# Optimization experiments

Measured on AMD Instinct MI355X. Metric: run time of the kernel, lower is better.

Reference implementation:

```python
import jax, jax.numpy as jnp
import numpy as np

EPS = 1e-6  # torch F.pairwise_distance eps, added to the difference elementwise

B, Z = 8192, 128
N_CLASSES = 62
P = int(N_CLASSES * 1.5)  # 93 proxies


def pdist(a, b):
    """||a_i - b_j + EPS||_2 for all pairs, without a [N,M,Z] intermediate.
    Expansion: ||a-b||^2 + 2*EPS*sum(a-b) + Z*EPS^2."""
    aa = jnp.sum(a * a, axis=-1)[:, None]
    bb = jnp.sum(b * b, axis=-1)[None, :]
    ab = a @ b.T
    eps_term = 2.0 * EPS * (jnp.sum(a, -1)[:, None] - jnp.sum(b, -1)[None, :]) + a.shape[-1] * EPS * EPS
    return jnp.sqrt(jnp.maximum(aa + bb - 2.0 * ab + eps_term, 0.0))


def setup_inputs() -> dict:
    key = jax.random.key(0)
    k0, k1, k2 = jax.random.split(key, 3)
    z = jax.random.normal(k0, (B, Z), dtype=jnp.float32)
    y_idx = jax.random.randint(k1, (B,), 0, N_CLASSES, dtype=jnp.int32)
    proxies = jax.random.uniform(k2, (P, Z), dtype=jnp.float32)  # nn.init.uniform_
    y_map = jnp.arange(N_CLASSES, dtype=jnp.int32)  # y_to_relative_y_train (unique classes)
    return {"z": z, "y_idx": y_idx, "proxies": proxies, "y_map": y_map}


def reference(z, y_idx, proxies, y_map):
    # F.normalize(proxies, p=2, dim=-1) with 1e-12 clamp
    prx = proxies / jnp.maximum(jnp.linalg.norm(proxies, axis=-1, keepdims=True), 1e-12)
    # y_rel[j] = position where y_to_relative_y_train == y_idx[j] (exactly one match)
    y_rel = jnp.argmax(y_map[None, :] == y_idx[:, None], axis=-1)  # [B]

    anchors = np.arange(0, z.shape[0] - 3, 3)  # static anchor indices i
    z_a = z[anchors]                            # [A,Z]

    # nearest proxy to each anchor
    D_prox = pdist(z_a, prx)                    # [A,P]
    prox_p = prx[jnp.argmin(D_prox, axis=-1)]   # [A,Z]

    # distance from chosen proxy to every sample; restrict to suffix j>=i with same class
    D_pz = pdist(prox_p, z)                     # [A,B]
    mask = (np.arange(z.shape[0])[None, :] >= anchors[:, None]) & \
           (y_rel[None, :] == y_rel[anchors][:, None])  # [A,B], row i always has j=i True
    D_pos = jnp.where(mask, D_pz, -jnp.inf)
    j_p = jnp.argmax(D_pos, axis=-1)            # hardest positive index
    D_p = jnp.take_along_axis(D_pos, j_p[:, None], axis=-1)[:, 0]  # [A]

    # distances from hardest positive to all proxies -> NCA denominator
    D_n = pdist(z[j_p], prx)                    # [A,P]
    losses = D_p + jax.nn.logsumexp(-D_n, axis=-1)  # -log(exp(-D_p)/sum exp(-D_n))
    return jnp.mean(losses)
```

## Files before the change

### kernel.cpp

```cpp
#include <hip/hip_runtime.h>
#include <math.h>

#define B_N   8192
#define Z_D   128
#define P_N   93
#define NCLS  62
#define A_N   2730
#define BCAP  256
#define GT_S  96
#define NPART 683
#define TWO_EPS   2e-6f
#define ZEPS2     (128.0f * 1e-6f * 1e-6f)

__device__ __forceinline__ float wave_sum(float v) {
#pragma unroll
  for (int off = 1; off < 64; off <<= 1) v += __shfl_xor(v, off, 64);
  return v;
}
__device__ __forceinline__ float wave_min(float v) {
#pragma unroll
  for (int off = 1; off < 64; off <<= 1) v = fminf(v, __shfl_xor(v, off, 64));
  return v;
}

__global__ __launch_bounds__(512) void kA(
    const float* __restrict__ z, const int* __restrict__ y_idx,
    const float* __restrict__ prox, const int* __restrict__ y_map,
    float* __restrict__ pp, float* __restrict__ sp,
    float* __restrict__ zz, float* __restrict__ sz,
    int* __restrict__ cnt, int2* __restrict__ bkt, float* __restrict__ GT) {
  __shared__ float linv[6];
  __shared__ int lmem[BCAP];
  __shared__ int lcnt;
  const int b = blockIdx.x, tid = threadIdx.x;
  const int lane = tid & 63, wv = tid >> 6;

  if (b < 256) {
    const int jch = b & 15, kt = b >> 4, k0 = kt * 6;
    const int nk = (kt == 15) ? 3 : 6;
    const int j = jch * 512 + tid;
    const float* __restrict__ zrow = z + (size_t)j * Z_D;
    if (wv < nk) {
      const int k = k0 + wv;
      const float a = prox[k * Z_D + lane];
      const float c = prox[k * Z_D + 64 + lane];
      const float s = wave_sum(a + c);
      const float q = wave_sum(a * a + c * c);
      const float inv = 1.0f / fmaxf(sqrtf(q), 1e-12f);
      if (lane == 0) {
        linv[wv] = inv;
        if (jch == 0) { pp[k] = q * inv * inv; sp[k] = s * inv; }
      }
    }
    __syncthreads();
    if (kt < 15) {
      const float* __restrict__ p0 = prox + (size_t)(k0 + 0) * Z_D;
      const float* __restrict__ p1 = prox + (size_t)(k0 + 1) * Z_D;
      const float* __restrict__ p2 = prox + (size_t)(k0 + 2) * Z_D;
      const float* __restrict__ p3 = prox + (size_t)(k0 + 3) * Z_D;
      const float* __restrict__ p4 = prox + (size_t)(k0 + 4) * Z_D;
      const float* __restrict__ p5 = prox + (size_t)(k0 + 5) * Z_D;
      float a0 = 0, a1 = 0, a2 = 0, a3 = 0, a4 = 0, a5 = 0;
#pragma unroll 8
      for (int i4 = 0; i4 < Z_D; i4 += 4) {
        const float4 zv = *(const float4*)(zrow + i4);
        const float4 q0 = *(const float4*)(p0 + i4);
        const float4 q1 = *(const float4*)(p1 + i4);
        const float4 q2 = *(const float4*)(p2 + i4);
        const float4 q3 = *(const float4*)(p3 + i4);
        const float4 q4 = *(const float4*)(p4 + i4);
        const float4 q5 = *(const float4*)(p5 + i4);
        a0 += zv.x * q0.x + zv.y * q0.y + zv.z * q0.z + zv.w * q0.w;
        a1 += zv.x * q1.x + zv.y * q1.y + zv.z * q1.z + zv.w * q1.w;
        a2 += zv.x * q2.x + zv.y * q2.y + zv.z * q2.z + zv.w * q2.w;
        a3 += zv.x * q3.x + zv.y * q3.y + zv.z * q3.z + zv.w * q3.w;
        a4 += zv.x * q4.x + zv.y * q4.y + zv.z * q4.z + zv.w * q4.w;
        a5 += zv.x * q5.x + zv.y * q5.y + zv.z * q5.z + zv.w * q5.w;
      }
      const float v0 = linv[0], v1 = linv[1], v2 = linv[2];
      const float v3 = linv[3], v4 = linv[4], v5 = linv[5];
      float* g = GT + (size_t)j * GT_S + k0;
      *(float2*)(g + 0) = make_float2(a0 * v0, a1 * v1);
      *(float2*)(g + 2) = make_float2(a2 * v2, a3 * v3);
      *(float2*)(g + 4) = make_float2(a4 * v4, a5 * v5);
    } else {
      const float* __restrict__ p0 = prox + (size_t)90 * Z_D;
      const float* __restrict__ p1 = prox + (size_t)91 * Z_D;
      const float* __restrict__ p2 = prox + (size_t)92 * Z_D;
      float a0 = 0, a1 = 0, a2 = 0, zs = 0, zq = 0;
#pragma unroll 8
      for (int i4 = 0; i4 < Z_D; i4 += 4) {
        const float4 zv = *(const float4*)(zrow + i4);
        const float4 q0 = *(const float4*)(p0 + i4);
        const float4 q1 = *(const float4*)(p1 + i4);
        const float4 q2 = *(const float4*)(p2 + i4);
        zs += zv.x + zv.y + zv.z + zv.w;
        zq += zv.x * zv.x + zv.y * zv.y + zv.z * zv.z + zv.w * zv.w;
        a0 += zv.x * q0.x + zv.y * q0.y + zv.z * q0.z + zv.w * q0.w;
        a1 += zv.x * q1.x + zv.y * q1.y + zv.z * q1.z + zv.w * q1.w;
        a2 += zv.x * q2.x + zv.y * q2.y + zv.z * q2.z + zv.w * q2.w;
      }
      float* g = GT + (size_t)j * GT_S + 90;
      *(float2*)(g) = make_float2(a0 * linv[0], a1 * linv[1]);
      g[2] = a2 * linv[2];
      zz[j] = zq;
      sz[j] = zs;
    }
  } else {
    const int c = b - 256;
    if (tid == 0) lcnt = 0;
    __syncthreads();
    const int ym = y_map[c];
    for (int j = tid; j < B_N; j += 512) {
      if (y_idx[j] == ym) {
        const int pos = atomicAdd(&lcnt, 1);
        if (pos < BCAP) lmem[pos] = j;
      }
    }
    __syncthreads();
    const int n = min(lcnt, BCAP);
    if (tid == 0) cnt[c] = n;
    for (int m = wv; m < n; m += 8) {
      const int j = lmem[m];
      const float a = z[(size_t)j * Z_D + lane];
      const float c2 = z[(size_t)j * Z_D + 64 + lane];
      const float s = wave_sum(a + c2);
      const float q = wave_sum(a * a + c2 * c2);
      if (lane == 0)
        bkt[c * BCAP + m] = make_int2(j, __float_as_int(q - TWO_EPS * s));
    }
  }
}

__global__ __launch_bounds__(256) void kB2(
    const int* __restrict__ y_idx, const int* __restrict__ y_map,
    const float* __restrict__ pp, const float* __restrict__ sp,
    const float* __restrict__ zz, const float* __restrict__ sz,
    const int* __restrict__ cnt, const int2* __restrict__ bkt,
    const float* __restrict__ GT, float* __restrict__ partial) {
  __shared__ float lpp[P_N], lsp[P_N];
  __shared__ int lymap[NCLS];
  __shared__ float part[4];
  const int tid = threadIdx.x, lane = tid & 63, wv = tid >> 6;
  if (tid < P_N) { lpp[tid] = pp[tid]; lsp[tid] = sp[tid]; }
  if (tid < NCLS) lymap[tid] = y_map[tid];
  __syncthreads();

  const int wid = blockIdx.x * 4 + wv;
  float loss = 0.0f;
  if (wid < A_N) {
    const int i = 3 * wid;
    const int yi = y_idx[i];
    const unsigned long long mm = __ballot(lane < NCLS && lymap[lane] == yi);
    const int cls = __ffsll(mm) - 1;
    const float zzi = zz[i], szi = sz[i];
    const int kB = lane + 64;

    const float* __restrict__ GTi = GT + (size_t)i * GT_S;
    float v1 = fmaxf(zzi + lpp[lane] - 2.0f * GTi[lane] +
                     TWO_EPS * (szi - lsp[lane]) + ZEPS2, 0.0f);
    int i1 = lane;
    if (kB < P_N) {
      const float v2 = fmaxf(zzi + lpp[kB] - 2.0f * GTi[kB] +
                             TWO_EPS * (szi - lsp[kB]) + ZEPS2, 0.0f);
      if (v2 < v1) { v1 = v2; i1 = kB; }
    }
#pragma unroll
    for (int off = 1; off < 64; off <<= 1) {
      const float ov = __shfl_xor(v1, off, 64);
      const int oi = __shfl_xor(i1, off, 64);
      if (ov < v1 || (ov == v1 && oi < i1)) { v1 = ov; i1 = oi; }
    }
    const int p = i1;

    const float cp = lpp[p] + TWO_EPS * lsp[p] + ZEPS2;
    const int n = cnt[cls];
    const int2* __restrict__ bk = bkt + cls * BCAP;
    float best = -INFINITY;
    int bestj = 0x7fffffff;
    for (int t = lane; t < n; t += 64) {
      const int2 e = bk[t];
      const int jj = e.x;
      if (jj >= i) {
        const float vv = fmaxf(cp + __int_as_float(e.y) -
                               2.0f * GT[(size_t)jj * GT_S + p], 0.0f);
        if (vv > best || (vv == best && jj < bestj)) { best = vv; bestj = jj; }
      }
    }
#pragma unroll
    for (int off = 1; off < 64; off <<= 1) {
      const float ov = __shfl_xor(best, off, 64);
      const int oj = __shfl_xor(bestj, off, 64);
      if (ov > best || (ov == best && oj < bestj)) { best = ov; bestj = oj; }
    }
    const float Dp = sqrtf(best);
    const int jp = bestj;

    const float zzj = zz[jp], szj = sz[jp];
    const float* __restrict__ GTj = GT + (size_t)jp * GT_S;
    const float d1 = sqrtf(fmaxf(zzj + lpp[lane] - 2.0f * GTj[lane] +
                                 TWO_EPS * (szj - lsp[lane]) + ZEPS2, 0.0f));
    float d2 = INFINITY;
    if (kB < P_N)
      d2 = sqrtf(fmaxf(zzj + lpp[kB] - 2.0f * GTj[kB] +
                       TWO_EPS * (szj - lsp[kB]) + ZEPS2, 0.0f));
    const float mn = wave_min(fminf(d1, d2));
    float ss = expf(mn - d1) + ((kB < P_N) ? expf(mn - d2) : 0.0f);
    ss = wave_sum(ss);
    loss = Dp - mn + logf(ss);
  }
  if (lane == 0) part[wv] = (wid < A_N) ? loss : 0.0f;
  __syncthreads();
  if (tid == 0)
    partial[blockIdx.x] = part[0] + part[1] + part[2] + part[3];
}

__global__ __launch_bounds__(256) void kC2(const float* __restrict__ partial,
                                           float* __restrict__ out) {
  __shared__ float ps[4];
  const int tid = threadIdx.x, lane = tid & 63, wv = tid >> 6;
  float s = 0.0f;
  for (int i = tid; i < NPART; i += 256) s += partial[i];
  s = wave_sum(s);
  if (lane == 0) ps[wv] = s;
  __syncthreads();
  if (tid == 0)
    out[0] = (ps[0] + ps[1] + ps[2] + ps[3]) * (1.0f / (float)A_N);
}

extern "C" void kernel_launch(void* const* d_in, const int* in_sizes, int n_in,
                              void* d_out, int out_size, void* d_ws, size_t ws_size,
                              hipStream_t stream) {
  const float* z = (const float*)d_in[0];
  const int* y_idx = (const int*)d_in[1];
  const float* prox = (const float*)d_in[2];
  const int* y_map = (const int*)d_in[3];
  float* out = (float*)d_out;

  char* ws = (char*)d_ws;
  float* pp    = (float*)(ws + 0);
  float* sp    = (float*)(ws + 512);
  float* zz    = (float*)(ws + 1024);
  float* sz    = (float*)(ws + 33792);
  int*   cnt   = (int*)  (ws + 66560);
  int2*  bkt   = (int2*) (ws + 66816);
  float* parts = (float*)(ws + 193792);
  float* GT    = (float*)(ws + 196608);

  kA<<<256 + NCLS, 512, 0, stream>>>(z, y_idx, prox, y_map,
                                     pp, sp, zz, sz, cnt, bkt, GT);
  kB2<<<NPART, 256, 0, stream>>>(y_idx, y_map, pp, sp, zz, sz,
                                 cnt, bkt, GT, parts);
  kC2<<<1, 256, 0, stream>>>(parts, out);
}
```

Baseline: 90.93 us.

## Fuse final reduction via atomics, 2 rows per thread in kA, prefetch bucket loads

Removes the third reduction kernel. kB2 blocks instead add their partial sums into a global accumulator, and the last block, found with an atomic counter, writes the mean. kA is halved to 256 threads with each thread computing two z rows, which reuses the proxy loads. The bucket scan in kB2 is unrolled into four prefetched loads so the GT gathers can overlap. This saves one launch and exposes more memory-level parallelism, but the float atomics make the summation order nondeterministic, and the accumulator is reset in kA, which relies on kernel ordering.

```diff
diff --git a/kernel.cpp b/kernel.cpp
--- a/kernel.cpp
+++ b/kernel.cpp
@@ -12,6 +12,9 @@
 #define TWO_EPS   2e-6f
 #define ZEPS2     (128.0f * 1e-6f * 1e-6f)
 
+#define AT_ADDU(p, v) __hip_atomic_fetch_add((p), (v), __ATOMIC_RELAXED, __HIP_MEMORY_SCOPE_AGENT)
+#define AT_ADDF(p, v) __hip_atomic_fetch_add((p), (v), __ATOMIC_RELAXED, __HIP_MEMORY_SCOPE_AGENT)
+
 __device__ __forceinline__ float wave_sum(float v) {
 #pragma unroll
   for (int off = 1; off < 64; off <<= 1) v += __shfl_xor(v, off, 64);
@@ -23,36 +26,40 @@
   return v;
 }
 
-__global__ __launch_bounds__(512) void kA(
+__global__ __launch_bounds__(256) void kA(
     const float* __restrict__ z, const int* __restrict__ y_idx,
     const float* __restrict__ prox, const int* __restrict__ y_map,
     float* __restrict__ pp, float* __restrict__ sp,
     float* __restrict__ zz, float* __restrict__ sz,
-    int* __restrict__ cnt, int2* __restrict__ bkt, float* __restrict__ GT) {
+    int* __restrict__ cnt, int2* __restrict__ bkt, float* __restrict__ GT,
+    float* __restrict__ accf, unsigned int* __restrict__ bar) {
   __shared__ float linv[6];
   __shared__ int lmem[BCAP];
   __shared__ int lcnt;
   const int b = blockIdx.x, tid = threadIdx.x;
   const int lane = tid & 63, wv = tid >> 6;
 
+  if (b == 0 && tid == 0) { accf[0] = 0.0f; bar[0] = 0u; }
+
   if (b < 256) {
     const int jch = b & 15, kt = b >> 4, k0 = kt * 6;
     const int nk = (kt == 15) ? 3 : 6;
-    const int j = jch * 512 + tid;
-    const float* __restrict__ zrow = z + (size_t)j * Z_D;
-    if (wv < nk) {
-      const int k = k0 + wv;
+    for (int r = wv; r < nk; r += 4) {
+      const int k = k0 + r;
       const float a = prox[k * Z_D + lane];
       const float c = prox[k * Z_D + 64 + lane];
       const float s = wave_sum(a + c);
       const float q = wave_sum(a * a + c * c);
       const float inv = 1.0f / fmaxf(sqrtf(q), 1e-12f);
       if (lane == 0) {
-        linv[wv] = inv;
+        linv[r] = inv;
         if (jch == 0) { pp[k] = q * inv * inv; sp[k] = s * inv; }
       }
     }
     __syncthreads();
+    const int j0 = jch * 512 + tid, j1 = j0 + 256;
+    const float* __restrict__ zr0 = z + (size_t)j0 * Z_D;
+    const float* __restrict__ zr1 = z + (size_t)j1 * Z_D;
     if (kt < 15) {
       const float* __restrict__ p0 = prox + (size_t)(k0 + 0) * Z_D;
       const float* __restrict__ p1 = prox + (size_t)(k0 + 1) * Z_D;
@@ -61,57 +68,79 @@
       const float* __restrict__ p4 = prox + (size_t)(k0 + 4) * Z_D;
       const float* __restrict__ p5 = prox + (size_t)(k0 + 5) * Z_D;
       float a0 = 0, a1 = 0, a2 = 0, a3 = 0, a4 = 0, a5 = 0;
+      float b0 = 0, b1 = 0, b2 = 0, b3 = 0, b4 = 0, b5 = 0;
 #pragma unroll 8
       for (int i4 = 0; i4 < Z_D; i4 += 4) {
-        const float4 zv = *(const float4*)(zrow + i4);
+        const float4 z0 = *(const float4*)(zr0 + i4);
+        const float4 z1 = *(const float4*)(zr1 + i4);
         const float4 q0 = *(const float4*)(p0 + i4);
         const float4 q1 = *(const float4*)(p1 + i4);
         const float4 q2 = *(const float4*)(p2 + i4);
         const float4 q3 = *(const float4*)(p3 + i4);
         const float4 q4 = *(const float4*)(p4 + i4);
         const float4 q5 = *(const float4*)(p5 + i4);
-        a0 += zv.x * q0.x + zv.y * q0.y + zv.z * q0.z + zv.w * q0.w;
-        a1 += zv.x * q1.x + zv.y * q1.y + zv.z * q1.z + zv.w * q1.w;
-        a2 += zv.x * q2.x + zv.y * q2.y + zv.z * q2.z + zv.w * q2.w;
-        a3 += zv.x * q3.x + zv.y * q3.y + zv.z * q3.z + zv.w * q3.w;
-        a4 += zv.x * q4.x + zv.y * q4.y + zv.z * q4.z + zv.w * q4.w;
-        a5 += zv.x * q5.x + zv.y * q5.y + zv.z * q5.z + zv.w * q5.w;
+        a0 += z0.x * q0.x + z0.y * q0.y + z0.z * q0.z + z0.w * q0.w;
+        a1 += z0.x * q1.x + z0.y * q1.y + z0.z * q1.z + z0.w * q1.w;
+        a2 += z0.x * q2.x + z0.y * q2.y + z0.z * q2.z + z0.w * q2.w;
+        a3 += z0.x * q3.x + z0.y * q3.y + z0.z * q3.z + z0.w * q3.w;
+        a4 += z0.x * q4.x + z0.y * q4.y + z0.z * q4.z + z0.w * q4.w;
+        a5 += z0.x * q5.x + z0.y * q5.y + z0.z * q5.z + z0.w * q5.w;
+        b0 += z1.x * q0.x + z1.y * q0.y + z1.z * q0.z + z1.w * q0.w;
+        b1 += z1.x * q1.x + z1.y * q1.y + z1.z * q1.z + z1.w * q1.w;
+        b2 += z1.x * q2.x + z1.y * q2.y + z1.z * q2.z + z1.w * q2.w;
+        b3 += z1.x * q3.x + z1.y * q3.y + z1.z * q3.z + z1.w * q3.w;
+        b4 += z1.x * q4.x + z1.y * q4.y + z1.z * q4.z + z1.w * q4.w;
+        b5 += z1.x * q5.x + z1.y * q5.y + z1.z * q5.z + z1.w * q5.w;
       }
       const float v0 = linv[0], v1 = linv[1], v2 = linv[2];
       const float v3 = linv[3], v4 = linv[4], v5 = linv[5];
-      float* g = GT + (size_t)j * GT_S + k0;
-      *(float2*)(g + 0) = make_float2(a0 * v0, a1 * v1);
-      *(float2*)(g + 2) = make_float2(a2 * v2, a3 * v3);
-      *(float2*)(g + 4) = make_float2(a4 * v4, a5 * v5);
+      float* g0 = GT + (size_t)j0 * GT_S + k0;
+      float* g1 = GT + (size_t)j1 * GT_S + k0;
+      *(float2*)(g0 + 0) = make_float2(a0 * v0, a1 * v1);
+      *(float2*)(g0 + 2) = make_float2(a2 * v2, a3 * v3);
+      *(float2*)(g0 + 4) = make_float2(a4 * v4, a5 * v5);
+      *(float2*)(g1 + 0) = make_float2(b0 * v0, b1 * v1);
+      *(float2*)(g1 + 2) = make_float2(b2 * v2, b3 * v3);
+      *(float2*)(g1 + 4) = make_float2(b4 * v4, b5 * v5);
     } else {
       const float* __restrict__ p0 = prox + (size_t)90 * Z_D;
       const float* __restrict__ p1 = prox + (size_t)91 * Z_D;
       const float* __restrict__ p2 = prox + (size_t)92 * Z_D;
-      float a0 = 0, a1 = 0, a2 = 0, zs = 0, zq = 0;
+      float a0 = 0, a1 = 0, a2 = 0, b0 = 0, b1 = 0, b2 = 0;
+      float s0 = 0, q0s = 0, s1 = 0, q1s = 0;
 #pragma unroll 8
       for (int i4 = 0; i4 < Z_D; i4 += 4) {
-        const float4 zv = *(const float4*)(zrow + i4);
+        const float4 z0 = *(const float4*)(zr0 + i4);
+        const float4 z1 = *(const float4*)(zr1 + i4);
         const float4 q0 = *(const float4*)(p0 + i4);
         const float4 q1 = *(const float4*)(p1 + i4);
         const float4 q2 = *(const float4*)(p2 + i4);
-        zs += zv.x + zv.y + zv.z + zv.w;
-        zq += zv.x * zv.x + zv.y * zv.y + zv.z * zv.z + zv.w * zv.w;
-        a0 += zv.x * q0.x + zv.y * q0.y + zv.z * q0.z + zv.w * q0.w;
-        a1 += zv.x * q1.x + zv.y * q1.y + zv.z * q1.z + zv.w * q1.w;
-        a2 += zv.x * q2.x + zv.y * q2.y + zv.z * q2.z + zv.w * q2.w;
-      }
-      float* g = GT + (size_t)j * GT_S + 90;
-      *(float2*)(g) = make_float2(a0 * linv[0], a1 * linv[1]);
-      g[2] = a2 * linv[2];
-      zz[j] = zq;
-      sz[j] = zs;
+        s0 += z0.x + z0.y + z0.z + z0.w;
+        q0s += z0.x * z0.x + z0.y * z0.y + z0.z * z0.z + z0.w * z0.w;
+        s1 += z1.x + z1.y + z1.z + z1.w;
+        q1s += z1.x * z1.x + z1.y * z1.y + z1.z * z1.z + z1.w * z1.w;
+        a0 += z0.x * q0.x + z0.y * q0.y + z0.z * q0.z + z0.w * q0.w;
+        a1 += z0.x * q1.x + z0.y * q1.y + z0.z * q1.z + z0.w * q1.w;
+        a2 += z0.x * q2.x + z0.y * q2.y + z0.z * q2.z + z0.w * q2.w;
+        b0 += z1.x * q0.x + z1.y * q0.y + z1.z * q0.z + z1.w * q0.w;
+        b1 += z1.x * q1.x + z1.y * q1.y + z1.z * q1.z + z1.w * q1.w;
+        b2 += z1.x * q2.x + z1.y * q2.y + z1.z * q2.z + z1.w * q2.w;
+      }
+      float* g0 = GT + (size_t)j0 * GT_S + 90;
+      float* g1 = GT + (size_t)j1 * GT_S + 90;
+      *(float2*)(g0) = make_float2(a0 * linv[0], a1 * linv[1]);
+      g0[2] = a2 * linv[2];
+      *(float2*)(g1) = make_float2(b0 * linv[0], b1 * linv[1]);
+      g1[2] = b2 * linv[2];
+      zz[j0] = q0s; sz[j0] = s0;
+      zz[j1] = q1s; sz[j1] = s1;
     }
   } else {
     const int c = b - 256;
     if (tid == 0) lcnt = 0;
     __syncthreads();
     const int ym = y_map[c];
-    for (int j = tid; j < B_N; j += 512) {
+    for (int j = tid; j < B_N; j += 256) {
       if (y_idx[j] == ym) {
         const int pos = atomicAdd(&lcnt, 1);
         if (pos < BCAP) lmem[pos] = j;
@@ -120,7 +149,7 @@
     __syncthreads();
     const int n = min(lcnt, BCAP);
     if (tid == 0) cnt[c] = n;
-    for (int m = wv; m < n; m += 8) {
+    for (int m = wv; m < n; m += 4) {
       const int j = lmem[m];
       const float a = z[(size_t)j * Z_D + lane];
       const float c2 = z[(size_t)j * Z_D + 64 + lane];
@@ -137,7 +166,8 @@
     const float* __restrict__ pp, const float* __restrict__ sp,
     const float* __restrict__ zz, const float* __restrict__ sz,
     const int* __restrict__ cnt, const int2* __restrict__ bkt,
-    const float* __restrict__ GT, float* __restrict__ partial) {
+    const float* __restrict__ GT, float* accf, unsigned int* bar,
+    float* __restrict__ out) {
   __shared__ float lpp[P_N], lsp[P_N];
   __shared__ int lymap[NCLS];
   __shared__ float part[4];
@@ -176,14 +206,25 @@
     const float cp = lpp[p] + TWO_EPS * lsp[p] + ZEPS2;
     const int n = cnt[cls];
     const int2* __restrict__ bk = bkt + cls * BCAP;
+    int2 e[4];
+    float gg[4];
+#pragma unroll
+    for (int r = 0; r < 4; ++r) {
+      const int t = lane + r * 64;
+      e[r] = (t < n) ? bk[t] : make_int2(-1, 0);
+    }
+#pragma unroll
+    for (int r = 0; r < 4; ++r) {
+      const int row = (e[r].x >= i) ? e[r].x : i;
+      gg[r] = GT[(size_t)row * GT_S + p];
+    }
     float best = -INFINITY;
     int bestj = 0x7fffffff;
-    for (int t = lane; t < n; t += 64) {
-      const int2 e = bk[t];
-      const int jj = e.x;
+#pragma unroll
+    for (int r = 0; r < 4; ++r) {
+      const int jj = e[r].x;
       if (jj >= i) {
-        const float vv = fmaxf(cp + __int_as_float(e.y) -
-                               2.0f * GT[(size_t)jj * GT_S + p], 0.0f);
+        const float vv = fmaxf(cp + __int_as_float(e[r].y) - 2.0f * gg[r], 0.0f);
         if (vv > best || (vv == best && jj < bestj)) { best = vv; bestj = jj; }
       }
     }
@@ -211,21 +252,14 @@
   }
   if (lane == 0) part[wv] = (wid < A_N) ? loss : 0.0f;
   __syncthreads();
-  if (tid == 0)
-    partial[blockIdx.x] = part[0] + part[1] + part[2] + part[3];
-}
-
-__global__ __launch_bounds__(256) void kC2(const float* __restrict__ partial,
-                                           float* __restrict__ out) {
-  __shared__ float ps[4];
-  const int tid = threadIdx.x, lane = tid & 63, wv = tid >> 6;
-  float s = 0.0f;
-  for (int i = tid; i < NPART; i += 256) s += partial[i];
-  s = wave_sum(s);
-  if (lane == 0) ps[wv] = s;
-  __syncthreads();
-  if (tid == 0)
-    out[0] = (ps[0] + ps[1] + ps[2] + ps[3]) * (1.0f / (float)A_N);
+
+  if (tid == 0) {
+    AT_ADDF(accf, part[0] + part[1] + part[2] + part[3]);
+    __builtin_amdgcn_s_waitcnt(0);
+    const unsigned old = AT_ADDU(bar, 1u);
+    if (old == (unsigned)(NPART - 1))
+      out[0] = AT_ADDF(accf, 0.0f) * (1.0f / (float)A_N);
+  }
 }
 
 extern "C" void kernel_launch(void* const* d_in, const int* in_sizes, int n_in,
@@ -238,18 +272,18 @@
   float* out = (float*)d_out;
 
   char* ws = (char*)d_ws;
-  float* pp    = (float*)(ws + 0);
-  float* sp    = (float*)(ws + 512);
-  float* zz    = (float*)(ws + 1024);
-  float* sz    = (float*)(ws + 33792);
-  int*   cnt   = (int*)  (ws + 66560);
-  int2*  bkt   = (int2*) (ws + 66816);
-  float* parts = (float*)(ws + 193792);
-  float* GT    = (float*)(ws + 196608);
-
-  kA<<<256 + NCLS, 512, 0, stream>>>(z, y_idx, prox, y_map,
-                                     pp, sp, zz, sz, cnt, bkt, GT);
+  float*        accf = (float*)(ws + 0);
+  unsigned int* bar  = (unsigned int*)(ws + 128);
+  float* pp    = (float*)(ws + 512);
+  float* sp    = (float*)(ws + 1024);
+  float* zz    = (float*)(ws + 1536);
+  float* sz    = (float*)(ws + 34304);
+  int*   cnt   = (int*)  (ws + 67072);
+  int2*  bkt   = (int2*) (ws + 67328);
+  float* GT    = (float*)(ws + 194304);
+
+  kA<<<256 + NCLS, 256, 0, stream>>>(z, y_idx, prox, y_map,
+                                     pp, sp, zz, sz, cnt, bkt, GT, accf, bar);
   kB2<<<NPART, 256, 0, stream>>>(y_idx, y_map, pp, sp, zz, sz,
-                                 cnt, bkt, GT, parts);
-  kC2<<<1, 256, 0, stream>>>(parts, out);
-}
+                                 cnt, bkt, GT, accf, bar, out);
+}
```

Result: slower. 112.7 us (+23.9%).
